# Kernel tuning notes

Measured on AMD Instinct MI355X. Metric: run time of the kernel, lower is better.

Reference implementation:

```python
import jax, jax.numpy as jnp
import numpy as np

C_IN, C_OUT, K, H, W = 16, 16, 3, 1024, 1024
PAD = 1  # 'same' padding for 3x3 stride-1


def setup_inputs() -> dict:
    key = jax.random.key(0)
    kx, kw, kb = jax.random.split(key, 3)
    x = jax.random.normal(kx, (1, C_IN, H, W), dtype=jnp.float32)
    weight = jax.random.normal(kw, (C_OUT, C_IN, K, K), dtype=jnp.float32) * 0.05
    bias = jax.random.normal(kb, (C_OUT,), dtype=jnp.float32) * 0.05
    return {"x": x, "weight": weight, "bias": bias}


def reference(x, weight, bias):
    # Original module: im2col (unfold) + matmul + reshape + bias add.
    # Mathematically identical to a dense 2D convolution (cross-correlation),
    # expressed here as the fused implicit-GEMM conv primitive.
    out = jax.lax.conv_general_dilated(
        x, weight,
        window_strides=(1, 1),
        padding=((PAD, PAD), (PAD, PAD)),
        dimension_numbers=("NCHW", "OIHW", "NCHW"),
    )  # [1, C_OUT, H, W]
    # out_unf.view(*output_shape) drops the batch dim (batch must be 1)
    return out[0] + bias[:, None, None]
```

## Files before the change

kernel.cpp:

```cpp
#include <hip/hip_runtime.h>


#define HH 1024
#define WW 1024
#define CIN 16
#define COUT 16
#define TW 64
#define TH 16
#define LROWS (TH + 2)
#define LCOLS (TW + 2)
#define PIX 16
#define NPIX (LROWS * LCOLS)

typedef short v8s __attribute__((ext_vector_type(8)));
typedef float v4f __attribute__((ext_vector_type(4)));
typedef unsigned int u32;

__device__ __forceinline__ unsigned short f32_bf16(float f) {
    union { float f; u32 u; } v;
    v.f = f;
    u32 u = v.u;
    u += 0x7fffu + ((u >> 16) & 1u);
    return (unsigned short)(u >> 16);
}

__global__ __launch_bounds__(256, 4)
void conv3x3_fused(const float* __restrict__ x,
                   const float* __restrict__ wgt,
                   const float* __restrict__ bias,
                   float* __restrict__ out) {
    __shared__ __align__(16) unsigned short sm[NPIX * PIX];

    const int tid = threadIdx.x;
    const int lane = tid & 63;
    const int wave = tid >> 6;
    const int h0 = blockIdx.y * TH;
    const int w0 = blockIdx.x * TW;

    #pragma unroll
    for (int i = 0; i < 5; ++i) {
        const int p = i * 256 + tid;
        if (p < NPIX) {
            const int r = p / LCOLS;
            const int col = p - r * LCOLS;
            const int gh = h0 - 1 + r;
            const int gw = w0 - 1 + col;
            float f[CIN];
            #pragma unroll
            for (int c = 0; c < CIN; ++c) f[c] = 0.0f;
            if ((unsigned)gh < (unsigned)HH && (unsigned)gw < (unsigned)WW) {
                const float* src = x + (size_t)gh * WW + gw;
                #pragma unroll
                for (int c = 0; c < CIN; ++c)
                    f[c] = src[(size_t)c * (HH * WW)];
            }
            u32 pk[8];
            #pragma unroll
            for (int c = 0; c < 8; ++c)
                pk[c] = (u32)f32_bf16(f[2 * c]) | ((u32)f32_bf16(f[2 * c + 1]) << 16);
            const int c0 = p * 2;
            const int sel = (c0 >> 3) & 1;
            uint4* dst = (uint4*)(sm + c0 * 8);
            dst[sel] = *(uint4*)&pk[0];
            dst[1 - sel] = *(uint4*)&pk[4];
        }
    }

    const int m = lane & 15;
    const int q = lane >> 4;
    const int colbase = wave * 16 + m;

    v8s a[5];
    int Kofs[5];
    #pragma unroll
    for (int g5 = 0; g5 < 5; ++g5) {
        int t = 4 * g5 + q;
        int tt = t > 17 ? 17 : t;
        int khkw = tt >> 1;
        int kh = khkw / 3;
        int kw = khkw - 3 * kh;
        int half = tt & 1;
        Kofs[g5] = (kh * LCOLS + colbase + kw) * 2 + half;
        bool valid = t < 18;
        #pragma unroll
        for (int j = 0; j < 8; ++j) {
            float wv = valid ? wgt[((m * CIN + half * 8 + j) * 3 + kh) * 3 + kw] : 0.0f;
            a[g5][j] = (short)f32_bf16(wv);
        }
    }
    float bl[4];
    #pragma unroll
    for (int i = 0; i < 4; ++i) bl[i] = bias[q * 4 + i];

    __syncthreads();

    #pragma unroll 4
    for (int r = 0; r < TH; ++r) {
        v4f acc = {0.f, 0.f, 0.f, 0.f};
        #pragma unroll
        for (int g5 = 0; g5 < 5; ++g5) {
            int c = r * (LCOLS * 2) + Kofs[g5];
            int phys = c ^ ((c >> 3) & 1);
            v8s b = *(const v8s*)(sm + phys * 8);
            acc = __builtin_amdgcn_mfma_f32_16x16x32_bf16(a[g5], b, acc, 0, 0, 0);
        }
        float* op = out + (size_t)(h0 + r) * WW + (w0 + colbase);
        #pragma unroll
        for (int i = 0; i < 4; ++i)
            op[(size_t)(q * 4 + i) * (HH * WW)] = acc[i] + bl[i];
    }
}

extern "C" void kernel_launch(void* const* d_in, const int* in_sizes, int n_in,
                              void* d_out, int out_size, void* d_ws, size_t ws_size,
                              hipStream_t stream) {
    const float* x = (const float*)d_in[0];
    const float* w = (const float*)d_in[1];
    const float* b = (const float*)d_in[2];
    float* out = (float*)d_out;
    dim3 grid(WW / TW, HH / TH);
    conv3x3_fused<<<grid, dim3(256), 0, stream>>>(x, w, b, out);
}
```

Measured before the change: 140.2 us.

## Vectorize input staging with float4 loads, separate halo path, widen LDS swizzle

The tile-staging loop now has each thread load four consecutive pixels per channel with float4 global loads for the interior 64 columns, instead of one scalar load per pixel. The left and right halo columns are handled by a separate scalar path on a subset of threads. The LDS XOR swizzle is widened from 1 bit to 3 bits so that the new write pattern and the MFMA operand reads spread across more banks. This targets global load instruction count and LDS bank conflicts, at the cost of more per-thread registers for the 16 float4 values and uneven work across threads.

```diff
diff --git a/kernel.cpp b/kernel.cpp
--- a/kernel.cpp
+++ b/kernel.cpp
@@ -24,6 +24,8 @@
     return (unsigned short)(u >> 16);
 }
 
+__device__ __forceinline__ int swz(int c) { return c ^ ((c >> 3) & 7); }
+
 __global__ __launch_bounds__(256, 4)
 void conv3x3_fused(const float* __restrict__ x,
                    const float* __restrict__ wgt,
@@ -37,34 +39,67 @@
     const int h0 = blockIdx.y * TH;
     const int w0 = blockIdx.x * TW;
 
-    #pragma unroll
-    for (int i = 0; i < 5; ++i) {
-        const int p = i * 256 + tid;
-        if (p < NPIX) {
-            const int r = p / LCOLS;
-            const int col = p - r * LCOLS;
-            const int gh = h0 - 1 + r;
-            const int gw = w0 - 1 + col;
-            float f[CIN];
+    auto stage_body = [&](int b) {
+        const int r = b >> 4;
+        const int j = b & 15;
+        const int gh = h0 - 1 + r;
+        const int pbase = r * LCOLS + 1 + 4 * j;
+        float4 f4[CIN];
+        if ((unsigned)gh < (unsigned)HH) {
+            const float4* src = (const float4*)(x + (size_t)gh * WW + w0) + j;
             #pragma unroll
-            for (int c = 0; c < CIN; ++c) f[c] = 0.0f;
-            if ((unsigned)gh < (unsigned)HH && (unsigned)gw < (unsigned)WW) {
-                const float* src = x + (size_t)gh * WW + gw;
-                #pragma unroll
-                for (int c = 0; c < CIN; ++c)
-                    f[c] = src[(size_t)c * (HH * WW)];
-            }
+            for (int c = 0; c < CIN; ++c)
+                f4[c] = src[(size_t)c * (HH * WW / 4)];
+        } else {
+            #pragma unroll
+            for (int c = 0; c < CIN; ++c)
+                f4[c] = make_float4(0.f, 0.f, 0.f, 0.f);
+        }
+        #pragma unroll
+        for (int k = 0; k < 4; ++k) {
             u32 pk[8];
             #pragma unroll
-            for (int c = 0; c < 8; ++c)
-                pk[c] = (u32)f32_bf16(f[2 * c]) | ((u32)f32_bf16(f[2 * c + 1]) << 16);
-            const int c0 = p * 2;
-            const int sel = (c0 >> 3) & 1;
-            uint4* dst = (uint4*)(sm + c0 * 8);
-            dst[sel] = *(uint4*)&pk[0];
-            dst[1 - sel] = *(uint4*)&pk[4];
+            for (int i = 0; i < 8; ++i) {
+                const float lo = ((const float*)&f4[2 * i])[k];
+                const float hi = ((const float*)&f4[2 * i + 1])[k];
+                pk[i] = (u32)f32_bf16(lo) | ((u32)f32_bf16(hi) << 16);
+            }
+            #pragma unroll
+            for (int half = 0; half < 2; ++half) {
+                const int cc = 2 * pbase + 2 * k + half;
+                *(uint4*)(sm + swz(cc) * 8) = *(uint4*)&pk[half * 4];
+            }
         }
-    }
+    };
+    auto stage_halo = [&](int h) {
+        const int r = h >> 1;
+        const int side = h & 1;
+        const int gh = h0 - 1 + r;
+        const int gw = side ? (w0 + 64) : (w0 - 1);
+        const int p = r * LCOLS + (side ? 65 : 0);
+        float f[CIN];
+        if ((unsigned)gh < (unsigned)HH && (unsigned)gw < (unsigned)WW) {
+            const float* src = x + (size_t)gh * WW + gw;
+            #pragma unroll
+            for (int c = 0; c < CIN; ++c) f[c] = src[(size_t)c * (HH * WW)];
+        } else {
+            #pragma unroll
+            for (int c = 0; c < CIN; ++c) f[c] = 0.f;
+        }
+        u32 pk[8];
+        #pragma unroll
+        for (int i = 0; i < 8; ++i)
+            pk[i] = (u32)f32_bf16(f[2 * i]) | ((u32)f32_bf16(f[2 * i + 1]) << 16);
+        #pragma unroll
+        for (int half = 0; half < 2; ++half) {
+            const int cc = 2 * p + half;
+            *(uint4*)(sm + swz(cc) * 8) = *(uint4*)&pk[half * 4];
+        }
+    };
+
+    stage_body(tid);
+    if (tid < 32) stage_body(256 + tid);
+    else if (tid < 68) stage_halo(tid - 32);
 
     const int m = lane & 15;
     const int q = lane >> 4;
@@ -100,8 +135,7 @@
         #pragma unroll
         for (int g5 = 0; g5 < 5; ++g5) {
             int c = r * (LCOLS * 2) + Kofs[g5];
-            int phys = c ^ ((c >> 3) & 1);
-            v8s b = *(const v8s*)(sm + phys * 8);
+            v8s b = *(const v8s*)(sm + swz(c) * 8);
             acc = __builtin_amdgcn_mfma_f32_16x16x32_bf16(a[g5], b, acc, 0, 0, 0);
         }
         float* op = out + (size_t)(h0 + r) * WW + (w0 + colbase);
```

Measured after the change: 132.1 us. 5.8% less time.
